# Kernel optimization log

Measured on AMD Instinct MI355X. Metric: run time of the kernel, lower is better.

Reference implementation:

```python
import jax, jax.numpy as jnp
import numpy as np

N, E, DIN, DH, DOUT = 100000, 1600000, 512, 128, 40


def setup_inputs() -> dict:
    key = jax.random.key(0)
    ks = jax.random.split(key, 4)
    x = jax.random.normal(ks[0], (N, DIN), dtype=jnp.float32)
    edge_index = jax.random.randint(ks[1], (2, E), 0, N, dtype=jnp.int32)
    W1 = jax.random.normal(ks[2], (DIN, DH), dtype=jnp.float32) / np.sqrt(DIN).astype(np.float32)
    b1 = jnp.zeros((DH,), jnp.float32)
    W2 = jax.random.normal(ks[3], (DH, DOUT), dtype=jnp.float32) / np.sqrt(DH).astype(np.float32)
    b2 = jnp.zeros((DOUT,), jnp.float32)
    return {"x": x, "edge_index": edge_index, "W1": W1, "b1": b1, "W2": W2, "b2": b2}


def _gcn_conv(x, W, b, src, dst, norm, n):
    # PyG GCNConv: linear transform first, then normalized neighbor aggregation
    h = x @ W                                   # [n, d_out]
    msg = h[src] * norm[:, None]                # gather + scale, [E+n, d_out]
    out = jax.ops.segment_sum(msg, dst, num_segments=n)  # scatter-add
    return out + b


def reference(x, edge_index, W1, b1, W2, b2):
    n = x.shape[0]
    loops = jnp.arange(n, dtype=edge_index.dtype)
    src = jnp.concatenate([edge_index[0], loops])   # with self-loops
    dst = jnp.concatenate([edge_index[1], loops])
    deg = jax.ops.segment_sum(jnp.ones_like(dst, dtype=jnp.float32), dst, num_segments=n)
    dinv = jnp.where(deg > 0, jax.lax.rsqrt(jnp.maximum(deg, 1.0)), 0.0)
    norm = dinv[src] * dinv[dst]                    # deg^{-1/2}[j] * deg^{-1/2}[i]
    h = jax.nn.relu(_gcn_conv(x, W1, b1, src, dst, norm, n))
    # dropout p=0.5 is a no-op in eval mode (training=False)
    h = _gcn_conv(h, W2, b2, src, dst, norm, n)
    return h, jax.nn.log_softmax(h, axis=1)
```

## Files before the change

### kernel.cpp

```cpp
#include <hip/hip_runtime.h>
#include <math.h>


typedef unsigned int uint;
typedef unsigned short ushort_t;
using short8  = __attribute__((ext_vector_type(8))) short;
using float4v = __attribute__((ext_vector_type(4))) float;

__device__ __forceinline__ ushort_t f2bf(float f) {
    uint u = __float_as_uint(f);
    u += 0x7FFFu + ((u >> 16) & 1u);
    return (ushort_t)(u >> 16);
}
__device__ __forceinline__ float2 unpack2(uint v) {
    return make_float2(__uint_as_float(v << 16), __uint_as_float(v & 0xFFFF0000u));
}
__device__ __forceinline__ uint pack2(float a, float b) {
    return (uint)f2bf(a) | ((uint)f2bf(b) << 16);
}
__device__ __forceinline__ void acc8(float* acc, uint4 v) {
    float2 a0 = unpack2(v.x), a1 = unpack2(v.y), a2 = unpack2(v.z), a3 = unpack2(v.w);
    acc[0] += a0.x; acc[1] += a0.y; acc[2] += a1.x; acc[3] += a1.y;
    acc[4] += a2.x; acc[5] += a2.y; acc[6] += a3.x; acc[7] += a3.y;
}
__device__ __forceinline__ void acc8s(float* acc, uint4 v, float d) {
    float2 a0 = unpack2(v.x), a1 = unpack2(v.y), a2 = unpack2(v.z), a3 = unpack2(v.w);
    acc[0] = fmaf(d, a0.x, acc[0]); acc[1] = fmaf(d, a0.y, acc[1]);
    acc[2] = fmaf(d, a1.x, acc[2]); acc[3] = fmaf(d, a1.y, acc[3]);
    acc[4] = fmaf(d, a2.x, acc[4]); acc[5] = fmaf(d, a2.y, acc[5]);
    acc[6] = fmaf(d, a3.x, acc[6]); acc[7] = fmaf(d, a3.y, acc[7]);
}

__device__ __forceinline__ void gemm1_block(int gb, const float* __restrict__ x,
                                            const ushort_t* __restrict__ W1t,
                                            ushort_t* __restrict__ h, int n) {
    __shared__ ushort_t As[64][72];
    __shared__ ushort_t Bs[128][72];
    const int tid  = threadIdx.x;
    const int w    = tid >> 6, lane = tid & 63;
    const int quad = lane >> 4, l16 = lane & 15;
    const int row0 = gb * 64;

    float4v acc[8];
#pragma unroll
    for (int i = 0; i < 8; i++) acc[i] = (float4v)0.f;

    const int ar  = tid >> 2;
    const int akq = (tid & 3) * 16;
    const int br  = tid >> 1;
    const int bkq = (tid & 1) * 32;
    const int agrow = row0 + ar;
    const float* xp0 = &x[(size_t)agrow * 512];
    const ushort_t* wp0 = &W1t[(size_t)br * 512];

    for (int kb = 0; kb < 512; kb += 64) {
#pragma unroll
        for (int j = 0; j < 4; j++) {
            float4 v = make_float4(0.f, 0.f, 0.f, 0.f);
            if (agrow < n) v = *(const float4*)(xp0 + kb + akq + j * 4);
            ushort4 b;
            b.x = f2bf(v.x); b.y = f2bf(v.y); b.z = f2bf(v.z); b.w = f2bf(v.w);
            *(ushort4*)&As[ar][akq + j * 4] = b;
        }
#pragma unroll
        for (int j = 0; j < 8; j++) {
            *(ushort4*)&Bs[br][bkq + j * 4] = *(const ushort4*)(wp0 + kb + bkq + j * 4);
        }
        __syncthreads();
#pragma unroll
        for (int ks = 0; ks < 64; ks += 32) {
            short8 a = *(const short8*)&As[w * 16 + l16][ks + quad * 8];
#pragma unroll
            for (int ct = 0; ct < 8; ct++) {
                short8 b = *(const short8*)&Bs[ct * 16 + l16][ks + quad * 8];
                acc[ct] = __builtin_amdgcn_mfma_f32_16x16x32_bf16(a, b, acc[ct], 0, 0, 0);
            }
        }
        __syncthreads();
    }
#pragma unroll
    for (int r = 0; r < 4; r++) {
        int grow = row0 + w * 16 + quad * 4 + r;
        if (grow >= n) continue;
#pragma unroll
        for (int ct = 0; ct < 8; ct++) {
            int col = ct * 16 + l16;
            h[(size_t)grow * 128 + col] = f2bf(acc[ct][r]);
        }
    }
}

__global__ __launch_bounds__(256) void k_d1(const int* __restrict__ dst,
                                            int* __restrict__ bcnt, int e, int nb, int nblkA,
                                            const float* __restrict__ W1,
                                            const float* __restrict__ W2,
                                            ushort_t* __restrict__ W1t,
                                            ushort_t* __restrict__ W2t) {
    if ((int)blockIdx.x >= nblkA) {
        int idx = ((int)blockIdx.x - nblkA) * 256 + threadIdx.x;
        if (idx < 65536) {
            int nn = idx >> 9, k = idx & 511;
            W1t[idx] = f2bf(W1[(size_t)k * 128 + nn]);
        } else if (idx < 71680) {
            int j = idx - 65536;
            int c = j >> 7, k = j & 127;
            W2t[j] = (c < 40) ? f2bf(W2[(size_t)k * 40 + c]) : (ushort_t)0;
        }
        return;
    }
    __shared__ int sh[800];
    for (int t = threadIdx.x; t < nb; t += 256) sh[t] = 0;
    __syncthreads();
    int ibase = blockIdx.x * 2560 + threadIdx.x;
#pragma unroll
    for (int j = 0; j < 10; j++) {
        int i = ibase + j * 256;
        if (i < e) atomicAdd(&sh[dst[i] >> 7], 1);
    }
    __syncthreads();
    for (int t = threadIdx.x; t < nb; t += 256) {
        int c = sh[t];
        if (c) atomicAdd(&bcnt[t], c);
    }
}

__global__ __launch_bounds__(256) void k_d2(const int* __restrict__ bcnt, int* __restrict__ bbase,
                                            int* __restrict__ bcur, int* __restrict__ row_ptr,
                                            int nb, int n, int e,
                                            const float* __restrict__ x,
                                            const ushort_t* __restrict__ W1t,
                                            ushort_t* __restrict__ h, int goff) {
    if (blockIdx.x > 0) {
        gemm1_block((int)blockIdx.x - 1 + goff, x, W1t, h, n);
        return;
    }
    __shared__ int sd[256];
    int t = threadIdx.x;
    int base = t * 4;
    int v[4];
#pragma unroll
    for (int j = 0; j < 4; j++) v[j] = (base + j < nb) ? bcnt[base + j] : 0;
    int s0 = v[0], s1 = s0 + v[1], s2 = s1 + v[2], s3 = s2 + v[3];
    sd[t] = s3;
    __syncthreads();
    for (int d = 1; d < 256; d <<= 1) {
        int xv = (t >= d) ? sd[t - d] : 0;
        __syncthreads();
        sd[t] += xv;
        __syncthreads();
    }
    int excl = sd[t] - s3;
    int pre0 = excl, pre1 = excl + s0, pre2 = excl + s1, pre3 = excl + s2;
    if (base + 0 < nb) { bbase[base + 0] = pre0; bcur[base + 0] = pre0; }
    if (base + 1 < nb) { bbase[base + 1] = pre1; bcur[base + 1] = pre1; }
    if (base + 2 < nb) { bbase[base + 2] = pre2; bcur[base + 2] = pre2; }
    if (base + 3 < nb) { bbase[base + 3] = pre3; bcur[base + 3] = pre3; }
    if (t == 255) bbase[nb] = excl + s3;
    if (t == 0) row_ptr[n] = e;
}

__global__ __launch_bounds__(256) void k_d3(const int* __restrict__ src, const int* __restrict__ dst,
                                            int* __restrict__ bcur, uint* __restrict__ pbuf,
                                            int e, int nb, int nblkA,
                                            const float* __restrict__ x,
                                            const ushort_t* __restrict__ W1t,
                                            ushort_t* __restrict__ h, int n, int goff) {
    if ((int)blockIdx.x >= nblkA) {
        gemm1_block((int)blockIdx.x - nblkA + goff, x, W1t, h, n);
        return;
    }
    __shared__ int sh[800];
    __shared__ int base_l[800];
    for (int t = threadIdx.x; t < nb; t += 256) sh[t] = 0;
    __syncthreads();
    uint pk[10]; int bk[10]; int lp[10];
    int ibase = blockIdx.x * 2560 + threadIdx.x;
#pragma unroll
    for (int j = 0; j < 10; j++) {
        int i = ibase + j * 256;
        bk[j] = -1;
        if (i < e) {
            int s = src[i], d = dst[i];
            int b = d >> 7;
            bk[j] = b;
            pk[j] = ((uint)(d & 127) << 25) | (uint)s;
            lp[j] = atomicAdd(&sh[b], 1);
        }
    }
    __syncthreads();
    for (int t = threadIdx.x; t < nb; t += 256) {
        int c = sh[t];
        base_l[t] = c ? atomicAdd(&bcur[t], c) : 0;
    }
    __syncthreads();
#pragma unroll
    for (int j = 0; j < 10; j++) {
        if (bk[j] >= 0) pbuf[base_l[bk[j]] + lp[j]] = pk[j];
    }
}

__global__ __launch_bounds__(256) void k_d4(const uint* __restrict__ pbuf,
                                            const int* __restrict__ bbase,
                                            float* __restrict__ dinv,
                                            int* __restrict__ row_ptr,
                                            int* __restrict__ es_src, int n, int nb,
                                            const float* __restrict__ x,
                                            const ushort_t* __restrict__ W1t,
                                            ushort_t* __restrict__ h, int goff) {
    if ((int)blockIdx.x >= nb) {
        gemm1_block((int)blockIdx.x - nb + goff, x, W1t, h, n);
        return;
    }
    __shared__ int cl[128];
    __shared__ int cur[128];
    const int b = blockIdx.x;
    const int tid = threadIdx.x;
    const int ebeg = bbase[b], eend = bbase[b + 1];
    const int m = eend - ebeg;
    if (tid < 128) cl[tid] = 0;
    __syncthreads();
    for (int i = tid; i < m; i += 256) {
        uint p = pbuf[ebeg + i];
        atomicAdd(&cl[p >> 25], 1);
    }
    __syncthreads();
    int own = (tid < 128) ? cl[tid] : 0;
    for (int d = 1; d < 128; d <<= 1) {
        int v = 0;
        if (tid < 128 && tid >= d) v = cl[tid - d];
        __syncthreads();
        if (tid < 128 && tid >= d) cl[tid] += v;
        __syncthreads();
    }
    if (tid < 128) {
        int excl = cl[tid] - own;
        int node = b * 128 + tid;
        if (node < n) {
            dinv[node] = rsqrtf((float)(own + 1));
            row_ptr[node] = ebeg + excl;
        }
        cur[tid] = excl;
    }
    __syncthreads();
    for (int i = tid; i < m; i += 256) {
        uint p = pbuf[ebeg + i];
        int dl = (int)(p >> 25);
        int pos = atomicAdd(&cur[dl], 1);
        es_src[ebeg + pos] = (int)(p & 0x1FFFFFFu);
    }
}

__global__ __launch_bounds__(256) void k_agg1(const uint* __restrict__ h,
                                              const int* __restrict__ row_ptr,
                                              const int* __restrict__ es_src,
                                              const float* __restrict__ dinv,
                                              const float* __restrict__ b1,
                                              uint* __restrict__ h1, int n) {
    const int tid  = threadIdx.x;
    const int w    = tid >> 6;
    const int node = blockIdx.x * 2 + (w >> 1);
    if (node >= n) return;
    const int half = w & 1;
    const int lane = tid & 63;
    const int g8   = lane >> 3;
    const int l8   = lane & 7;
    const int k0 = row_ptr[node], k1 = row_ptr[node + 1];
    const float di = dinv[node];
    const uint ubase = half * 32 + l8 * 4;

    uint4 sv = *(const uint4*)&h[(size_t)node * 64 + ubase];

    float acc[8];
#pragma unroll
    for (int i = 0; i < 8; i++) acc[i] = 0.f;

    int k = k0 + g8;
    for (; k + 8 < k1; k += 16) {
        int s0 = es_src[k];
        int s1 = es_src[k + 8];
        float d0 = dinv[s0], d1 = dinv[s1];
        uint4 v0 = *(const uint4*)&h[(size_t)s0 * 64 + ubase];
        uint4 v1 = *(const uint4*)&h[(size_t)s1 * 64 + ubase];
        acc8s(acc, v0, d0);
        acc8s(acc, v1, d1);
    }
    for (; k < k1; k += 8) {
        int s0 = es_src[k];
        float d0 = dinv[s0];
        uint4 v0 = *(const uint4*)&h[(size_t)s0 * 64 + ubase];
        acc8s(acc, v0, d0);
    }

#pragma unroll
    for (int i = 0; i < 8; i++) {
        acc[i] += __shfl_xor(acc[i], 8);
        acc[i] += __shfl_xor(acc[i], 16);
        acc[i] += __shfl_xor(acc[i], 32);
    }
    acc8s(acc, sv, di);

    const int cbase = half * 64 + l8 * 8;
    float4 ba = *(const float4*)&b1[cbase];
    float4 bb = *(const float4*)&b1[cbase + 4];
    float r[8];
    r[0] = di * acc[0] + ba.x; r[1] = di * acc[1] + ba.y;
    r[2] = di * acc[2] + ba.z; r[3] = di * acc[3] + ba.w;
    r[4] = di * acc[4] + bb.x; r[5] = di * acc[5] + bb.y;
    r[6] = di * acc[6] + bb.z; r[7] = di * acc[7] + bb.w;
#pragma unroll
    for (int i = 0; i < 8; i++) r[i] = r[i] > 0.f ? r[i] : 0.f;

    if (g8 == 0) {
        uint4 o;
        o.x = pack2(r[0], r[1]); o.y = pack2(r[2], r[3]);
        o.z = pack2(r[4], r[5]); o.w = pack2(r[6], r[7]);
        *(uint4*)&h1[(size_t)node * 64 + ubase] = o;
    }
}

__global__ __launch_bounds__(256) void k_gemm2(const ushort_t* __restrict__ h1,
                                               const ushort_t* __restrict__ W2t,
                                               const float* __restrict__ dinv,
                                               ushort_t* __restrict__ g, int n) {
    __shared__ ushort_t As[64][136];
    __shared__ ushort_t Bs[48][136];
    const int tid  = threadIdx.x;
    const int w    = tid >> 6, lane = tid & 63;
    const int quad = lane >> 4, l16 = lane & 15;
    const int row0 = blockIdx.x * 64;

    {
        int ar = tid >> 2;
        int ak = (tid & 3) * 32;
        int grow = row0 + ar;
#pragma unroll
        for (int j = 0; j < 4; j++) {
            uint4 v = make_uint4(0, 0, 0, 0);
            if (grow < n) v = *(const uint4*)&h1[(size_t)grow * 128 + ak + j * 8];
            *(uint4*)&As[ar][ak + j * 8] = v;
        }
    }
    for (int i = tid; i < 768; i += 256) {
        int row = i >> 4, q = i & 15;
        *(uint4*)&Bs[row][q * 8] = *(const uint4*)&W2t[(size_t)row * 128 + q * 8];
    }
    __syncthreads();

    float4v acc[3];
#pragma unroll
    for (int i = 0; i < 3; i++) acc[i] = (float4v)0.f;
#pragma unroll
    for (int ks = 0; ks < 128; ks += 32) {
        short8 a = *(const short8*)&As[w * 16 + l16][ks + quad * 8];
#pragma unroll
        for (int ct = 0; ct < 3; ct++) {
            short8 b = *(const short8*)&Bs[ct * 16 + l16][ks + quad * 8];
            acc[ct] = __builtin_amdgcn_mfma_f32_16x16x32_bf16(a, b, acc[ct], 0, 0, 0);
        }
    }
#pragma unroll
    for (int r = 0; r < 4; r++) {
        int grow = row0 + w * 16 + quad * 4 + r;
        if (grow >= n) continue;
        float di = dinv[grow];
#pragma unroll
        for (int ct = 0; ct < 3; ct++) {
            int col = ct * 16 + l16;
            g[(size_t)grow * 64 + col] = f2bf(di * acc[ct][r]);
        }
        g[(size_t)grow * 64 + 48 + l16] = (ushort_t)0;
    }
}

__global__ __launch_bounds__(256) void k_agg2(const uint* __restrict__ g,
                                              const int* __restrict__ row_ptr,
                                              const int* __restrict__ es_src,
                                              const float* __restrict__ dinv,
                                              const float* __restrict__ b2,
                                              float* __restrict__ out1,
                                              float* __restrict__ out2, int n) {
    const int tid  = threadIdx.x;
    const int node = blockIdx.x * 4 + (tid >> 6);
    if (node >= n) return;
    const int lane = tid & 63;
    const int g8   = lane >> 3;
    const int l8   = lane & 7;
    const int k0 = row_ptr[node], k1 = row_ptr[node + 1];

    uint4 sv = *(const uint4*)&g[(size_t)node * 32 + l8 * 4];

    float acc[8];
#pragma unroll
    for (int i = 0; i < 8; i++) acc[i] = 0.f;

    int k = k0 + g8;
    for (; k + 8 < k1; k += 16) {
        int s0 = es_src[k];
        int s1 = es_src[k + 8];
        uint4 v0 = *(const uint4*)&g[(size_t)s0 * 32 + l8 * 4];
        uint4 v1 = *(const uint4*)&g[(size_t)s1 * 32 + l8 * 4];
        acc8(acc, v0);
        acc8(acc, v1);
    }
    for (; k < k1; k += 8) {
        int s0 = es_src[k];
        uint4 v0 = *(const uint4*)&g[(size_t)s0 * 32 + l8 * 4];
        acc8(acc, v0);
    }

#pragma unroll
    for (int i = 0; i < 8; i++) {
        acc[i] += __shfl_xor(acc[i], 8);
        acc[i] += __shfl_xor(acc[i], 16);
        acc[i] += __shfl_xor(acc[i], 32);
    }
    acc8(acc, sv);

    const float di = dinv[node];
    float v[8];
    if (l8 < 5) {
        float4 ba = *(const float4*)&b2[l8 * 8];
        float4 bb = *(const float4*)&b2[l8 * 8 + 4];
        v[0] = di * acc[0] + ba.x; v[1] = di * acc[1] + ba.y;
        v[2] = di * acc[2] + ba.z; v[3] = di * acc[3] + ba.w;
        v[4] = di * acc[4] + bb.x; v[5] = di * acc[5] + bb.y;
        v[6] = di * acc[6] + bb.z; v[7] = di * acc[7] + bb.w;
    } else {
#pragma unroll
        for (int i = 0; i < 8; i++) v[i] = 0.f;
    }

    float m = -1e30f;
    if (l8 < 5) {
#pragma unroll
        for (int i = 0; i < 8; i++) m = fmaxf(m, v[i]);
    }
#pragma unroll
    for (int d = 1; d < 8; d <<= 1) m = fmaxf(m, __shfl_xor(m, d));
    float s = 0.f;
    if (l8 < 5) {
#pragma unroll
        for (int i = 0; i < 8; i++) s += expf(v[i] - m);
    }
#pragma unroll
    for (int d = 1; d < 8; d <<= 1) s += __shfl_xor(s, d);
    float ls = logf(s) + m;

    if (l8 < 5) {
        if (g8 == 0) {
            *(float4*)&out1[(size_t)node * 40 + l8 * 8]     = make_float4(v[0], v[1], v[2], v[3]);
            *(float4*)&out1[(size_t)node * 40 + l8 * 8 + 4] = make_float4(v[4], v[5], v[6], v[7]);
        } else if (g8 == 1) {
            *(float4*)&out2[(size_t)node * 40 + l8 * 8] =
                make_float4(v[0] - ls, v[1] - ls, v[2] - ls, v[3] - ls);
            *(float4*)&out2[(size_t)node * 40 + l8 * 8 + 4] =
                make_float4(v[4] - ls, v[5] - ls, v[6] - ls, v[7] - ls);
        }
    }
}

static inline size_t align4(size_t v) { return (v + 3) & ~(size_t)3; }

extern "C" void kernel_launch(void* const* d_in, const int* in_sizes, int n_in,
                              void* d_out, int out_size, void* d_ws, size_t ws_size,
                              hipStream_t stream) {
    const float* x  = (const float*)d_in[0];
    const int*   ei = (const int*)d_in[1];
    const float* W1 = (const float*)d_in[2];
    const float* b1 = (const float*)d_in[3];
    const float* W2 = (const float*)d_in[4];
    const float* b2 = (const float*)d_in[5];

    const int n = in_sizes[0] / 512;
    const int e = in_sizes[1] / 2;
    const int* src = ei;
    const int* dst = ei + e;
    const int NB = (n + 127) >> 7;

    char* p = (char*)d_ws;
    int*      bcnt    = (int*)p;        p += align4(NB) * 4;
    int*      bbase   = (int*)p;        p += align4(NB + 1) * 4;
    int*      bcur    = (int*)p;        p += align4(NB) * 4;
    int*      row_ptr = (int*)p;        p += align4(n + 1) * 4;
    float*    dinv    = (float*)p;      p += align4(n) * 4;
    uint*     pbuf    = (uint*)p;       p += align4(e) * 4;
    int*      es_src  = (int*)p;        p += align4(e) * 4;
    ushort_t* W1t     = (ushort_t*)p;   p += (size_t)128 * 512 * 2;
    ushort_t* W2t     = (ushort_t*)p;   p += (size_t)48 * 128 * 2;
    ushort_t* h       = (ushort_t*)p;   p += (size_t)n * 128 * 2;
    ushort_t* h1      = (ushort_t*)p;   p += (size_t)n * 128 * 2;
    ushort_t* g       = h;
    float*    out1    = (float*)d_out;
    float*    out2    = out1 + (size_t)n * 40;

    const int B = 256;
    const int nblkA = (e + 2559) / 2560;
    const int NG = (n + 63) / 64;
    const int c  = (NG + 2) / 3;
    const int c2 = NG - 2 * c;

    hipMemsetAsync(bcnt, 0, (size_t)NB * 4, stream);

    k_d1<<<nblkA + 280, B, 0, stream>>>(dst, bcnt, e, NB, nblkA, W1, W2, W1t, W2t);
    k_d2<<<1 + c, B, 0, stream>>>(bcnt, bbase, bcur, row_ptr, NB, n, e, x, W1t, h, 0);
    k_d3<<<nblkA + c, B, 0, stream>>>(src, dst, bcur, pbuf, e, NB, nblkA, x, W1t, h, n, c);
    k_d4<<<NB + c2, B, 0, stream>>>(pbuf, bbase, dinv, row_ptr, es_src, n, NB, x, W1t, h, 2 * c);

    k_agg1<<<(n + 1) / 2, B, 0, stream>>>((const uint*)h, row_ptr, es_src, dinv, b1, (uint*)h1, n);

    k_gemm2<<<(n + 63) / 64, B, 0, stream>>>(h1, W2t, dinv, g, n);
    k_agg2<<<(n + 3) / 4, B, 0, stream>>>((const uint*)g, row_ptr, es_src, dinv, b2, out1, out2, n);
}
```

Measured before the change: 538.6 us.

## Slice feature matrices into 16-column panels for cache-resident aggregation

GEMM outputs are now stored as column-sliced panels (16 bf16 columns per slice, contiguous over nodes), and both aggregation kernels process one slice at a time across all nodes, so each slice's gather working set (about 3.2 MB) can stay in cache. The second aggregation writes pre-softmax logits to a scratch buffer, and a separate log-softmax kernel produces both outputs. In exchange, row pointers and edge lists are re-read once per slice, each gather moves only 4 bytes per lane, and there is an extra kernel launch plus a round trip through the scratch buffer.

```diff
diff --git a/kernel.cpp b/kernel.cpp
--- a/kernel.cpp
+++ b/kernel.cpp
@@ -18,28 +18,17 @@
 __device__ __forceinline__ uint pack2(float a, float b) {
     return (uint)f2bf(a) | ((uint)f2bf(b) << 16);
 }
-__device__ __forceinline__ void acc8(float* acc, uint4 v) {
-    float2 a0 = unpack2(v.x), a1 = unpack2(v.y), a2 = unpack2(v.z), a3 = unpack2(v.w);
-    acc[0] += a0.x; acc[1] += a0.y; acc[2] += a1.x; acc[3] += a1.y;
-    acc[4] += a2.x; acc[5] += a2.y; acc[6] += a3.x; acc[7] += a3.y;
-}
-__device__ __forceinline__ void acc8s(float* acc, uint4 v, float d) {
-    float2 a0 = unpack2(v.x), a1 = unpack2(v.y), a2 = unpack2(v.z), a3 = unpack2(v.w);
-    acc[0] = fmaf(d, a0.x, acc[0]); acc[1] = fmaf(d, a0.y, acc[1]);
-    acc[2] = fmaf(d, a1.x, acc[2]); acc[3] = fmaf(d, a1.y, acc[3]);
-    acc[4] = fmaf(d, a2.x, acc[4]); acc[5] = fmaf(d, a2.y, acc[5]);
-    acc[6] = fmaf(d, a3.x, acc[6]); acc[7] = fmaf(d, a3.y, acc[7]);
-}
 
 __device__ __forceinline__ void gemm1_block(int gb, const float* __restrict__ x,
                                             const ushort_t* __restrict__ W1t,
-                                            ushort_t* __restrict__ h, int n) {
+                                            ushort_t* __restrict__ hs, int n) {
     __shared__ ushort_t As[64][72];
     __shared__ ushort_t Bs[128][72];
     const int tid  = threadIdx.x;
     const int w    = tid >> 6, lane = tid & 63;
     const int quad = lane >> 4, l16 = lane & 15;
     const int row0 = gb * 64;
+    const size_t n16 = (size_t)n * 16;
 
     float4v acc[8];
 #pragma unroll
@@ -84,8 +73,7 @@
         if (grow >= n) continue;
 #pragma unroll
         for (int ct = 0; ct < 8; ct++) {
-            int col = ct * 16 + l16;
-            h[(size_t)grow * 128 + col] = f2bf(acc[ct][r]);
+            hs[(size_t)ct * n16 + (size_t)grow * 16 + l16] = f2bf(acc[ct][r]);
         }
     }
 }
@@ -129,9 +117,9 @@
                                             int nb, int n, int e,
                                             const float* __restrict__ x,
                                             const ushort_t* __restrict__ W1t,
-                                            ushort_t* __restrict__ h, int goff) {
+                                            ushort_t* __restrict__ hs, int goff) {
     if (blockIdx.x > 0) {
-        gemm1_block((int)blockIdx.x - 1 + goff, x, W1t, h, n);
+        gemm1_block((int)blockIdx.x - 1 + goff, x, W1t, hs, n);
         return;
     }
     __shared__ int sd[256];
@@ -164,9 +152,9 @@
                                             int e, int nb, int nblkA,
                                             const float* __restrict__ x,
                                             const ushort_t* __restrict__ W1t,
-                                            ushort_t* __restrict__ h, int n, int goff) {
+                                            ushort_t* __restrict__ hs, int n, int goff) {
     if ((int)blockIdx.x >= nblkA) {
-        gemm1_block((int)blockIdx.x - nblkA + goff, x, W1t, h, n);
+        gemm1_block((int)blockIdx.x - nblkA + goff, x, W1t, hs, n);
         return;
     }
     __shared__ int sh[800];
@@ -206,9 +194,9 @@
                                             int* __restrict__ es_src, int n, int nb,
                                             const float* __restrict__ x,
                                             const ushort_t* __restrict__ W1t,
-                                            ushort_t* __restrict__ h, int goff) {
+                                            ushort_t* __restrict__ hs, int goff) {
     if ((int)blockIdx.x >= nb) {
-        gemm1_block((int)blockIdx.x - nb + goff, x, W1t, h, n);
+        gemm1_block((int)blockIdx.x - nb + goff, x, W1t, hs, n);
         return;
     }
     __shared__ int cl[128];
@@ -250,84 +238,73 @@
     }
 }
 
-__global__ __launch_bounds__(256) void k_agg1(const uint* __restrict__ h,
-                                              const int* __restrict__ row_ptr,
-                                              const int* __restrict__ es_src,
-                                              const float* __restrict__ dinv,
-                                              const float* __restrict__ b1,
-                                              uint* __restrict__ h1, int n) {
+__global__ __launch_bounds__(256) void k_agg1s(const ushort_t* __restrict__ hs,
+                                               const int* __restrict__ row_ptr,
+                                               const int* __restrict__ es_src,
+                                               const float* __restrict__ dinv,
+                                               const float* __restrict__ b1,
+                                               uint* __restrict__ h1, int n, int sb) {
     const int tid  = threadIdx.x;
-    const int w    = tid >> 6;
-    const int node = blockIdx.x * 2 + (w >> 1);
-    if (node >= n) return;
-    const int half = w & 1;
+    const int wv   = tid >> 6;
     const int lane = tid & 63;
     const int g8   = lane >> 3;
     const int l8   = lane & 7;
-    const int k0 = row_ptr[node], k1 = row_ptr[node + 1];
-    const float di = dinv[node];
-    const uint ubase = half * 32 + l8 * 4;
-
-    uint4 sv = *(const uint4*)&h[(size_t)node * 64 + ubase];
-
-    float acc[8];
-#pragma unroll
-    for (int i = 0; i < 8; i++) acc[i] = 0.f;
-
-    int k = k0 + g8;
-    for (; k + 8 < k1; k += 16) {
-        int s0 = es_src[k];
-        int s1 = es_src[k + 8];
-        float d0 = dinv[s0], d1 = dinv[s1];
-        uint4 v0 = *(const uint4*)&h[(size_t)s0 * 64 + ubase];
-        uint4 v1 = *(const uint4*)&h[(size_t)s1 * 64 + ubase];
-        acc8s(acc, v0, d0);
-        acc8s(acc, v1, d1);
-    }
-    for (; k < k1; k += 8) {
-        int s0 = es_src[k];
-        float d0 = dinv[s0];
-        uint4 v0 = *(const uint4*)&h[(size_t)s0 * 64 + ubase];
-        acc8s(acc, v0, d0);
-    }
-
-#pragma unroll
-    for (int i = 0; i < 8; i++) {
-        acc[i] += __shfl_xor(acc[i], 8);
-        acc[i] += __shfl_xor(acc[i], 16);
-        acc[i] += __shfl_xor(acc[i], 32);
-    }
-    acc8s(acc, sv, di);
-
-    const int cbase = half * 64 + l8 * 8;
-    float4 ba = *(const float4*)&b1[cbase];
-    float4 bb = *(const float4*)&b1[cbase + 4];
-    float r[8];
-    r[0] = di * acc[0] + ba.x; r[1] = di * acc[1] + ba.y;
-    r[2] = di * acc[2] + ba.z; r[3] = di * acc[3] + ba.w;
-    r[4] = di * acc[4] + bb.x; r[5] = di * acc[5] + bb.y;
-    r[6] = di * acc[6] + bb.z; r[7] = di * acc[7] + bb.w;
-#pragma unroll
-    for (int i = 0; i < 8; i++) r[i] = r[i] > 0.f ? r[i] : 0.f;
-
-    if (g8 == 0) {
-        uint4 o;
-        o.x = pack2(r[0], r[1]); o.y = pack2(r[2], r[3]);
-        o.z = pack2(r[4], r[5]); o.w = pack2(r[6], r[7]);
-        *(uint4*)&h1[(size_t)node * 64 + ubase] = o;
+    const int s    = blockIdx.x / sb;
+    const int nb0  = (blockIdx.x % sb) * 16 + wv * 4;
+    const uint* hp = (const uint*)(hs + (size_t)s * (size_t)n * 16);
+    const float bb0 = b1[s * 16 + l8 * 2];
+    const float bb1 = b1[s * 16 + l8 * 2 + 1];
+
+    for (int i = 0; i < 4; i++) {
+        const int node = nb0 + i;
+        if (node >= n) return;
+        const int k0 = row_ptr[node], k1 = row_ptr[node + 1];
+        const float di = dinv[node];
+        uint sv = hp[(size_t)node * 8 + l8];
+
+        float ax = 0.f, ay = 0.f;
+        int k = k0 + g8;
+        for (; k + 8 < k1; k += 16) {
+            int s0 = __builtin_nontemporal_load(&es_src[k]);
+            int s1 = __builtin_nontemporal_load(&es_src[k + 8]);
+            float d0 = dinv[s0], d1 = dinv[s1];
+            uint u0 = hp[(size_t)s0 * 8 + l8];
+            uint u1 = hp[(size_t)s1 * 8 + l8];
+            float2 f0 = unpack2(u0), f1 = unpack2(u1);
+            ax = fmaf(d0, f0.x, ax); ay = fmaf(d0, f0.y, ay);
+            ax = fmaf(d1, f1.x, ax); ay = fmaf(d1, f1.y, ay);
+        }
+        for (; k < k1; k += 8) {
+            int s0 = __builtin_nontemporal_load(&es_src[k]);
+            float d0 = dinv[s0];
+            float2 f0 = unpack2(hp[(size_t)s0 * 8 + l8]);
+            ax = fmaf(d0, f0.x, ax); ay = fmaf(d0, f0.y, ay);
+        }
+        ax += __shfl_xor(ax, 8);  ay += __shfl_xor(ay, 8);
+        ax += __shfl_xor(ax, 16); ay += __shfl_xor(ay, 16);
+        ax += __shfl_xor(ax, 32); ay += __shfl_xor(ay, 32);
+        float2 sf = unpack2(sv);
+        ax = fmaf(di, sf.x, ax); ay = fmaf(di, sf.y, ay);
+
+        float r0 = di * ax + bb0;
+        float r1 = di * ay + bb1;
+        r0 = r0 > 0.f ? r0 : 0.f;
+        r1 = r1 > 0.f ? r1 : 0.f;
+        if (g8 == 0) h1[(size_t)node * 64 + s * 8 + l8] = pack2(r0, r1);
     }
 }
 
 __global__ __launch_bounds__(256) void k_gemm2(const ushort_t* __restrict__ h1,
                                                const ushort_t* __restrict__ W2t,
                                                const float* __restrict__ dinv,
-                                               ushort_t* __restrict__ g, int n) {
+                                               ushort_t* __restrict__ gs, int n) {
     __shared__ ushort_t As[64][136];
     __shared__ ushort_t Bs[48][136];
     const int tid  = threadIdx.x;
     const int w    = tid >> 6, lane = tid & 63;
     const int quad = lane >> 4, l16 = lane & 15;
     const int row0 = blockIdx.x * 64;
+    const size_t n16 = (size_t)n * 16;
 
     {
         int ar = tid >> 2;
@@ -365,97 +342,86 @@
         float di = dinv[grow];
 #pragma unroll
         for (int ct = 0; ct < 3; ct++) {
-            int col = ct * 16 + l16;
-            g[(size_t)grow * 64 + col] = f2bf(di * acc[ct][r]);
-        }
-        g[(size_t)grow * 64 + 48 + l16] = (ushort_t)0;
-    }
-}
-
-__global__ __launch_bounds__(256) void k_agg2(const uint* __restrict__ g,
-                                              const int* __restrict__ row_ptr,
-                                              const int* __restrict__ es_src,
-                                              const float* __restrict__ dinv,
-                                              const float* __restrict__ b2,
+            gs[(size_t)ct * n16 + (size_t)grow * 16 + l16] = f2bf(di * acc[ct][r]);
+        }
+    }
+}
+
+__global__ __launch_bounds__(256) void k_agg2s(const ushort_t* __restrict__ gs,
+                                               const int* __restrict__ row_ptr,
+                                               const int* __restrict__ es_src,
+                                               const float* __restrict__ dinv,
+                                               const float* __restrict__ b2,
+                                               float* __restrict__ z, int n, int sb) {
+    const int tid  = threadIdx.x;
+    const int wv   = tid >> 6;
+    const int lane = tid & 63;
+    const int g8   = lane >> 3;
+    const int l8   = lane & 7;
+    const int s    = blockIdx.x / sb;
+    const int nb0  = (blockIdx.x % sb) * 16 + wv * 4;
+    const uint* gp = (const uint*)(gs + (size_t)s * (size_t)n * 16);
+    const int col0 = s * 16 + l8 * 2;
+    const float bb0 = (col0     < 40) ? b2[col0]     : 0.f;
+    const float bb1 = (col0 + 1 < 40) ? b2[col0 + 1] : 0.f;
+
+    for (int i = 0; i < 4; i++) {
+        const int node = nb0 + i;
+        if (node >= n) return;
+        const int k0 = row_ptr[node], k1 = row_ptr[node + 1];
+        const float di = dinv[node];
+        uint sv = gp[(size_t)node * 8 + l8];
+
+        float ax = 0.f, ay = 0.f;
+        int k = k0 + g8;
+        for (; k + 8 < k1; k += 16) {
+            int s0 = __builtin_nontemporal_load(&es_src[k]);
+            int s1 = __builtin_nontemporal_load(&es_src[k + 8]);
+            uint u0 = gp[(size_t)s0 * 8 + l8];
+            uint u1 = gp[(size_t)s1 * 8 + l8];
+            float2 f0 = unpack2(u0), f1 = unpack2(u1);
+            ax += f0.x + f1.x;
+            ay += f0.y + f1.y;
+        }
+        for (; k < k1; k += 8) {
+            int s0 = __builtin_nontemporal_load(&es_src[k]);
+            float2 f0 = unpack2(gp[(size_t)s0 * 8 + l8]);
+            ax += f0.x;
+            ay += f0.y;
+        }
+        ax += __shfl_xor(ax, 8);  ay += __shfl_xor(ay, 8);
+        ax += __shfl_xor(ax, 16); ay += __shfl_xor(ay, 16);
+        ax += __shfl_xor(ax, 32); ay += __shfl_xor(ay, 32);
+        float2 sf = unpack2(sv);
+        ax += sf.x; ay += sf.y;
+
+        float v0 = di * ax + bb0;
+        float v1 = di * ay + bb1;
+        if (g8 == 0) *(float2*)&z[(size_t)node * 48 + col0] = make_float2(v0, v1);
+    }
+}
+
+__global__ __launch_bounds__(256) void k_smax(const float* __restrict__ z,
                                               float* __restrict__ out1,
                                               float* __restrict__ out2, int n) {
     const int tid  = threadIdx.x;
     const int node = blockIdx.x * 4 + (tid >> 6);
     if (node >= n) return;
     const int lane = tid & 63;
-    const int g8   = lane >> 3;
-    const int l8   = lane & 7;
-    const int k0 = row_ptr[node], k1 = row_ptr[node + 1];
-
-    uint4 sv = *(const uint4*)&g[(size_t)node * 32 + l8 * 4];
-
-    float acc[8];
-#pragma unroll
-    for (int i = 0; i < 8; i++) acc[i] = 0.f;
-
-    int k = k0 + g8;
-    for (; k + 8 < k1; k += 16) {
-        int s0 = es_src[k];
-        int s1 = es_src[k + 8];
-        uint4 v0 = *(const uint4*)&g[(size_t)s0 * 32 + l8 * 4];
-        uint4 v1 = *(const uint4*)&g[(size_t)s1 * 32 + l8 * 4];
-        acc8(acc, v0);
-        acc8(acc, v1);
-    }
-    for (; k < k1; k += 8) {
-        int s0 = es_src[k];
-        uint4 v0 = *(const uint4*)&g[(size_t)s0 * 32 + l8 * 4];
-        acc8(acc, v0);
-    }
-
-#pragma unroll
-    for (int i = 0; i < 8; i++) {
-        acc[i] += __shfl_xor(acc[i], 8);
-        acc[i] += __shfl_xor(acc[i], 16);
-        acc[i] += __shfl_xor(acc[i], 32);
-    }
-    acc8(acc, sv);
-
-    const float di = dinv[node];
-    float v[8];
-    if (l8 < 5) {
-        float4 ba = *(const float4*)&b2[l8 * 8];
-        float4 bb = *(const float4*)&b2[l8 * 8 + 4];
-        v[0] = di * acc[0] + ba.x; v[1] = di * acc[1] + ba.y;
-        v[2] = di * acc[2] + ba.z; v[3] = di * acc[3] + ba.w;
-        v[4] = di * acc[4] + bb.x; v[5] = di * acc[5] + bb.y;
-        v[6] = di * acc[6] + bb.z; v[7] = di * acc[7] + bb.w;
-    } else {
-#pragma unroll
-        for (int i = 0; i < 8; i++) v[i] = 0.f;
-    }
-
-    float m = -1e30f;
-    if (l8 < 5) {
-#pragma unroll
-        for (int i = 0; i < 8; i++) m = fmaxf(m, v[i]);
-    }
-#pragma unroll
-    for (int d = 1; d < 8; d <<= 1) m = fmaxf(m, __shfl_xor(m, d));
-    float s = 0.f;
-    if (l8 < 5) {
-#pragma unroll
-        for (int i = 0; i < 8; i++) s += expf(v[i] - m);
-    }
-#pragma unroll
-    for (int d = 1; d < 8; d <<= 1) s += __shfl_xor(s, d);
-    float ls = logf(s) + m;
-
-    if (l8 < 5) {
-        if (g8 == 0) {
-            *(float4*)&out1[(size_t)node * 40 + l8 * 8]     = make_float4(v[0], v[1], v[2], v[3]);
-            *(float4*)&out1[(size_t)node * 40 + l8 * 8 + 4] = make_float4(v[4], v[5], v[6], v[7]);
-        } else if (g8 == 1) {
-            *(float4*)&out2[(size_t)node * 40 + l8 * 8] =
-                make_float4(v[0] - ls, v[1] - ls, v[2] - ls, v[3] - ls);
-            *(float4*)&out2[(size_t)node * 40 + l8 * 8 + 4] =
-                make_float4(v[4] - ls, v[5] - ls, v[6] - ls, v[7] - ls);
-        }
+
+    float v = (lane < 40) ? z[(size_t)node * 48 + lane] : -1e30f;
+    float m = v;
+#pragma unroll
+    for (int d = 1; d < 64; d <<= 1) m = fmaxf(m, __shfl_xor(m, d));
+    float ex = (lane < 40) ? expf(v - m) : 0.f;
+    float ssum = ex;
+#pragma unroll
+    for (int d = 1; d < 64; d <<= 1) ssum += __shfl_xor(ssum, d);
+    float ls = logf(ssum) + m;
+
+    if (lane < 40) {
+        out1[(size_t)node * 40 + lane] = v;
+        out2[(size_t)node * 40 + lane] = v - ls;
     }
 }
 
@@ -487,9 +453,10 @@
     int*      es_src  = (int*)p;        p += align4(e) * 4;
     ushort_t* W1t     = (ushort_t*)p;   p += (size_t)128 * 512 * 2;
     ushort_t* W2t     = (ushort_t*)p;   p += (size_t)48 * 128 * 2;
-    ushort_t* h       = (ushort_t*)p;   p += (size_t)n * 128 * 2;
+    ushort_t* hs      = (ushort_t*)p;   p += (size_t)n * 128 * 2;
     ushort_t* h1      = (ushort_t*)p;   p += (size_t)n * 128 * 2;
-    ushort_t* g       = h;
+    ushort_t* gs      = (ushort_t*)p;   p += (size_t)n * 48 * 2;
+    float*    z       = (float*)p;      p += (size_t)n * 48 * 4;
     float*    out1    = (float*)d_out;
     float*    out2    = out1 + (size_t)n * 40;
 
@@ -498,16 +465,18 @@
     const int NG = (n + 63) / 64;
     const int c  = (NG + 2) / 3;
     const int c2 = NG - 2 * c;
+    const int SB = (n + 15) >> 4;
 
     hipMemsetAsync(bcnt, 0, (size_t)NB * 4, stream);
 
     k_d1<<<nblkA + 280, B, 0, stream>>>(dst, bcnt, e, NB, nblkA, W1, W2, W1t, W2t);
-    k_d2<<<1 + c, B, 0, stream>>>(bcnt, bbase, bcur, row_ptr, NB, n, e, x, W1t, h, 0);
-    k_d3<<<nblkA + c, B, 0, stream>>>(src, dst, bcur, pbuf, e, NB, nblkA, x, W1t, h, n, c);
-    k_d4<<<NB + c2, B, 0, stream>>>(pbuf, bbase, dinv, row_ptr, es_src, n, NB, x, W1t, h, 2 * c);
-
-    k_agg1<<<(n + 1) / 2, B, 0, stream>>>((const uint*)h, row_ptr, es_src, dinv, b1, (uint*)h1, n);
-
-    k_gemm2<<<(n + 63) / 64, B, 0, stream>>>(h1, W2t, dinv, g, n);
-    k_agg2<<<(n + 3) / 4, B, 0, stream>>>((const uint*)g, row_ptr, es_src, dinv, b2, out1, out2, n);
-}
+    k_d2<<<1 + c, B, 0, stream>>>(bcnt, bbase, bcur, row_ptr, NB, n, e, x, W1t, hs, 0);
+    k_d3<<<nblkA + c, B, 0, stream>>>(src, dst, bcur, pbuf, e, NB, nblkA, x, W1t, hs, n, c);
+    k_d4<<<NB + c2, B, 0, stream>>>(pbuf, bbase, dinv, row_ptr, es_src, n, NB, x, W1t, hs, 2 * c);
+
+    k_agg1s<<<8 * SB, B, 0, stream>>>(hs, row_ptr, es_src, dinv, b1, (uint*)h1, n, SB);
+
+    k_gemm2<<<(n + 63) / 64, B, 0, stream>>>(h1, W2t, dinv, gs, n);
+    k_agg2s<<<3 * SB, B, 0, stream>>>(gs, row_ptr, es_src, dinv, b2, z, n, SB);
+    k_smax<<<(n + 3) / 4, B, 0, stream>>>(z, out1, out2, n);
+}
```

Result: slower. 788.9 us (+46.5%).
